# Optimization experiments

Measured on AMD Instinct MI355X. Metric: run time of the kernel, lower is better.

## Reference

```python
import jax, jax.numpy as jnp
from jax import lax
import numpy as np

B, N, S, K = 8, 4096, 1024, 32
D_FEAT = 64
EPS = 1e-5


def fps_idx(pts, npoint):
    # pts: [N,3] -> farthest point sampling indices [npoint] (deterministic start at 0)
    n = pts.shape[0]
    def body(i, state):
        dist, far, idxs = state
        idxs = idxs.at[i].set(far)
        d = jnp.sum((pts - pts[far]) ** 2, axis=-1)
        dist = jnp.minimum(dist, d)
        return dist, jnp.argmax(dist).astype(jnp.int32), idxs
    init = (jnp.full((n,), 1e10, pts.dtype), jnp.int32(0), jnp.zeros((npoint,), jnp.int32))
    _, _, idxs = lax.fori_loop(0, npoint, body, init)
    return idxs


def bn(x, g, b, axes, c_axis):
    # batch-norm, training mode (batch statistics), matching torch default module state
    m = jnp.mean(x, axes, keepdims=True)
    v = jnp.var(x, axes, keepdims=True)
    shape = [1] * x.ndim
    shape[c_axis] = -1
    return g.reshape(shape) * (x - m) * lax.rsqrt(v + EPS) + b.reshape(shape)


def conv1x1(x, w, b):
    # x: [B,C,S,K], w: [O,C], b: [O]
    return jnp.einsum('oc,bcsk->bosk', w, x) + b[None, :, None, None]


def setup_inputs():
    key = jax.random.key(0)
    ks = jax.random.split(key, 20)
    p = lambda k, shape: jax.random.normal(k, shape, jnp.float32) * 0.05
    inp = {
        'xyz': jax.random.normal(ks[0], (B, 3, N), jnp.float32),
        'features': jax.random.normal(ks[1], (B, D_FEAT, N), jnp.float32),
        # main MLP: 67 -> 64 -> 64 -> 128
        'w0': p(ks[2], (64, 67)), 'b0': p(ks[3], (64,)), 'g0': jnp.ones(64), 'be0': jnp.zeros(64),
        'w1': p(ks[4], (64, 64)), 'b1': p(ks[5], (64,)), 'g1': jnp.ones(64), 'be1': jnp.zeros(64),
        'w2': p(ks[6], (128, 64)), 'b2': p(ks[7], (128,)), 'g2': jnp.ones(128), 'be2': jnp.zeros(128),
        # WeightNet: 3 -> 8 -> 8 -> 16
        'ww0': p(ks[8], (8, 3)), 'wb0': p(ks[9], (8,)), 'wg0': jnp.ones(8), 'wbe0': jnp.zeros(8),
        'ww1': p(ks[10], (8, 8)), 'wb1': p(ks[11], (8,)), 'wg1': jnp.ones(8), 'wbe1': jnp.zeros(8),
        'ww2': p(ks[12], (16, 8)), 'wb2': p(ks[13], (16,)), 'wg2': jnp.ones(16), 'wbe2': jnp.zeros(16),
        # final linear 16*128 -> 128 and BN1d
        'lw': p(ks[14], (128, 16 * 128)), 'lb': p(ks[15], (128,)),
        'lg': jnp.ones(128), 'lbe': jnp.zeros(128),
    }
    return inp


def reference(xyz, features, w0, b0, g0, be0, w1, b1, g1, be1, w2, b2, g2, be2,
              ww0, wb0, wg0, wbe0, ww1, wb1, wg1, wbe1, ww2, wb2, wg2, wbe2,
              lw, lb, lg, lbe):
    xyz_t = jnp.transpose(xyz, (0, 2, 1))          # [B,N,3]
    feat_t = jnp.transpose(features, (0, 2, 1))    # [B,N,D]

    # farthest point sampling (indices non-differentiable, as in CUDA FPS)
    fidx = jax.vmap(lambda pts: fps_idx(pts, S))(lax.stop_gradient(xyz_t))  # [B,S]
    fps_xyz = jnp.take_along_axis(xyz_t, fidx[..., None], axis=1)           # [B,S,3]

    # KNN: squared distances [B,S,N], take K smallest
    d2 = (jnp.sum(fps_xyz ** 2, -1, keepdims=True)
          + jnp.sum(xyz_t ** 2, -1)[:, None, :]
          - 2.0 * jnp.einsum('bsc,bnc->bsn', fps_xyz, xyz_t))
    _, idx = lax.top_k(-lax.stop_gradient(d2), K)                            # [B,S,K]

    gather = jax.vmap(lambda src, i: src[i])
    grouped_xyz = gather(xyz_t, idx) - fps_xyz[:, :, None, :]                # [B,S,K,3]
    grouped_feat = gather(feat_t, idx)                                       # [B,S,K,D]
    nf = jnp.concatenate([grouped_xyz, grouped_feat], axis=-1)               # [B,S,K,3+D]

    nf = jnp.transpose(nf, (0, 3, 1, 2))                                     # [B,C,S,K]
    for w, b, g, be in ((w0, b0, g0, be0), (w1, b1, g1, be1), (w2, b2, g2, be2)):
        nf = jax.nn.relu(bn(conv1x1(nf, w, b), g, be, (0, 2, 3), 1))

    gx = jnp.transpose(grouped_xyz, (0, 3, 1, 2))                            # [B,3,S,K]
    wts = gx
    for w, b, g, be in ((ww0, wb0, wg0, wbe0), (ww1, wb1, wg1, wbe1), (ww2, wb2, wg2, wbe2)):
        wts = jax.nn.relu(bn(conv1x1(wts, w, b), g, be, (0, 2, 3), 1))       # [B,16,S,K]

    agg = jnp.einsum('bdsk,bcsk->bsdc', nf, wts)                             # [B,S,128,16]
    agg = agg.reshape(agg.shape[0], agg.shape[1], -1)                        # [B,S,2048] (D outer, C inner)
    lin = agg @ lw.T + lb                                                    # [B,S,128]
    lin = jnp.transpose(lin, (0, 2, 1))                                      # [B,128,S]
    out_f = jax.nn.relu(bn(lin, lg, lbe, (0, 2), 1))

    new_xyz = jnp.transpose(fps_xyz, (0, 2, 1))                              # [B,3,S]
    return (new_xyz, out_f)
```

## Files before the change

### kernel.cpp

```cpp
#include <hip/hip_runtime.h>
#include <hip/hip_bf16.h>

#define BB 8
#define NN 4096
#define SS 1024
#define KK 32
#define PP (BB*SS*KK)

typedef unsigned long long u64;
typedef unsigned int u32;
typedef unsigned short u16;
typedef float f32x2 __attribute__((ext_vector_type(2)));
typedef float f32x4 __attribute__((ext_vector_type(4)));
typedef short bf16x8 __attribute__((ext_vector_type(8)));

#define ST_Y0 0
#define ST_W0 64
#define ST_Y1 72
#define ST_W1 136
#define ST_Y2 144
#define ST_W2 272
#define ST_LIN 288

static __device__ __forceinline__ float bf2f(u32 u){ return __uint_as_float(u<<16); }
static __device__ __forceinline__ u16 f2bf(float f){ u32 u=__float_as_uint(f); return (u16)((u + 0x7FFFu + ((u>>16)&1u))>>16); }

static __device__ __forceinline__ f32x2 pk_add(f32x2 a, f32x2 b){
  f32x2 d; asm("v_pk_add_f32 %0, %1, %2" : "=v"(d) : "v"(a), "v"(b)); return d;
}
static __device__ __forceinline__ f32x2 pk_mul(f32x2 a, f32x2 b){
  f32x2 d; asm("v_pk_mul_f32 %0, %1, %2" : "=v"(d) : "v"(a), "v"(b)); return d;
}

static __device__ __forceinline__ f32x4 mfma16(bf16x8 a, bf16x8 b, f32x4 c){
  return __builtin_amdgcn_mfma_f32_16x16x32_bf16(a,b,c,0,0,0);
}

static __device__ __forceinline__ uint4 pack8(const float* v){
  uint4 r;
  r.x=(u32)f2bf(v[0])|((u32)f2bf(v[1])<<16);
  r.y=(u32)f2bf(v[2])|((u32)f2bf(v[3])<<16);
  r.z=(u32)f2bf(v[4])|((u32)f2bf(v[5])<<16);
  r.w=(u32)f2bf(v[6])|((u32)f2bf(v[7])<<16);
  return r;
}

static __device__ __forceinline__ void unp8_aff(uint4 r, const float* A, const float* C, int cb, float* o){
  o[0]=fmaxf(fmaf(bf2f(r.x&0xffffu),A[cb+0],C[cb+0]),0.f);
  o[1]=fmaxf(fmaf(bf2f(r.x>>16)    ,A[cb+1],C[cb+1]),0.f);
  o[2]=fmaxf(fmaf(bf2f(r.y&0xffffu),A[cb+2],C[cb+2]),0.f);
  o[3]=fmaxf(fmaf(bf2f(r.y>>16)    ,A[cb+3],C[cb+3]),0.f);
  o[4]=fmaxf(fmaf(bf2f(r.z&0xffffu),A[cb+4],C[cb+4]),0.f);
  o[5]=fmaxf(fmaf(bf2f(r.z>>16)    ,A[cb+5],C[cb+5]),0.f);
  o[6]=fmaxf(fmaf(bf2f(r.w&0xffffu),A[cb+6],C[cb+6]),0.f);
  o[7]=fmaxf(fmaf(bf2f(r.w>>16)    ,A[cb+7],C[cb+7]),0.f);
}

template<int CTRL, int RMASK>
static __device__ __forceinline__ u32 dppmax(u32 m){
  u32 t=(u32)__builtin_amdgcn_update_dpp(0, (int)m, CTRL, RMASK, 0xf, false);
  return t>m ? t : m;
}
template<int CTRL, int RMASK>
static __device__ __forceinline__ float dppadd1(float v){
  float t=__uint_as_float((u32)__builtin_amdgcn_update_dpp(0,(int)__float_as_uint(v),CTRL,RMASK,0xf,false));
  return v+t;
}
static __device__ __forceinline__ float dppsum(float v){
  v=dppadd1<0x111,0xf>(v);
  v=dppadd1<0x112,0xf>(v);
  v=dppadd1<0x114,0xf>(v);
  v=dppadd1<0x118,0xf>(v);
  v=dppadd1<0x142,0xa>(v);
  v=dppadd1<0x143,0xc>(v);
  return v;
}
static __device__ __forceinline__ float rl63(float v){
  return __uint_as_float((u32)__builtin_amdgcn_readlane((int)__float_as_uint(v),63));
}

__global__ __launch_bounds__(256) void k_featT(const float* __restrict__ f, float* __restrict__ ft,
    const float* __restrict__ w0,const float* __restrict__ ww0,
    float* __restrict__ w0t,float* __restrict__ wt0,float* __restrict__ wt1,float* __restrict__ wt2,
    const float* __restrict__ ww1,const float* __restrict__ ww2,
    float* __restrict__ statsf){
  __shared__ float tile[64][65];
  if (blockIdx.x==512){
    int t=threadIdx.x;
    for (int i=t;i<1024;i+=256) statsf[i]=0.f;
    for (int i=t;i<64*67;i+=256){ int o=i/67,k=i%67; w0t[k*64+o]=w0[i]; }
    for (int i=t;i<8*3;i+=256){ int o=i/3,k=i%3; wt0[k*8+o]=ww0[i]; }
    for (int i=t;i<8*8;i+=256){ int o=i>>3,k=i&7; wt1[k*8+o]=ww1[i]; }
    for (int i=t;i<16*8;i+=256){ int o=i>>3,k=i&7; wt2[k*16+o]=ww2[i]; }
    return;
  }
  int b=blockIdx.x>>6; int n0=(blockIdx.x&63)*64;
  const float* fb=f+(size_t)b*64*NN;
  int c0=threadIdx.x>>6, nn=threadIdx.x&63;
  #pragma unroll
  for (int it=0;it<16;it++){ int c=c0+it*4; tile[c][nn]=fb[(size_t)c*NN+n0+nn]; }
  __syncthreads();
  int cc=threadIdx.x&63, n1=threadIdx.x>>6;
  float* fo=ft+((size_t)b*NN+n0)*64;
  #pragma unroll
  for (int it=0;it<16;it++){ int n=n1+it*4; fo[(size_t)n*64+cc]=tile[cc][n]; }
}

__global__ __launch_bounds__(512) void k_fps(const float* __restrict__ xyz,
                                             float* __restrict__ fpsq, float* __restrict__ outx){
  __shared__ float X[NN], Y[NN], Z[NN];
  __shared__ float QX[SS], QY[SS], QZ[SS];
  __shared__ u64 red[2][8];
  int b=blockIdx.x, t=threadIdx.x;
  const float* xb=xyz+(size_t)b*3*NN;
  for (int i=t;i<NN;i+=512){ X[i]=xb[i]; Y[i]=xb[NN+i]; Z[i]=xb[2*NN+i]; }
  __syncthreads();
  f32x2 px[4],py[4],pz[4],dd[4];
  #pragma unroll
  for (int k=0;k<4;k++){
    int i=t*8+2*k;
    px[k].x=X[i]; px[k].y=X[i+1];
    py[k].x=Y[i]; py[k].y=Y[i+1];
    pz[k].x=Z[i]; pz[k].y=Z[i+1];
    dd[k].x=1e10f; dd[k].y=1e10f;
  }
  int wv=t>>6, ln=t&63;
  int far=0;
  for (int s=0;s<SS;s++){
    float fx=X[far], fy=Y[far], fz=Z[far];
    if (t==0){ QX[s]=fx; QY[s]=fy; QZ[s]=fz; }
    f32x2 nfx, nfy, nfz;
    nfx.x=-fx; nfx.y=-fx; nfy.x=-fy; nfy.y=-fy; nfz.x=-fz; nfz.y=-fz;
    #pragma unroll
    for (int k=0;k<4;k++){
      f32x2 dx=pk_add(px[k],nfx);
      f32x2 xx=pk_mul(dx,dx);
      f32x2 dy=pk_add(py[k],nfy);
      f32x2 yy=pk_mul(dy,dy);
      f32x2 dz=pk_add(pz[k],nfz);
      f32x2 zz=pk_mul(dz,dz);
      f32x2 s1=pk_add(xx,yy);
      f32x2 d2=pk_add(s1,zz);
      dd[k].x=fminf(dd[k].x,d2.x);
      dd[k].y=fminf(dd[k].y,d2.y);
    }
    float m01=fmaxf(dd[0].x,dd[0].y), m23=fmaxf(dd[1].x,dd[1].y);
    float m45=fmaxf(dd[2].x,dd[2].y), m67=fmaxf(dd[3].x,dd[3].y);
    u32 m=__float_as_uint(fmaxf(fmaxf(m01,m23),fmaxf(m45,m67)));
    m=dppmax<0x111,0xf>(m);
    m=dppmax<0x112,0xf>(m);
    m=dppmax<0x114,0xf>(m);
    m=dppmax<0x118,0xf>(m);
    u32 r15=(u32)__builtin_amdgcn_readlane((int)m,15);
    u32 r31=(u32)__builtin_amdgcn_readlane((int)m,31);
    u32 r47=(u32)__builtin_amdgcn_readlane((int)m,47);
    u32 r63=(u32)__builtin_amdgcn_readlane((int)m,63);
    u32 ab = r15>r31 ? r15 : r31;
    u32 cd = r47>r63 ? r47 : r63;
    u32 wmax = ab>cd ? ab : cd;
    int lj=8;
    if (__float_as_uint(dd[3].y)==wmax) lj=7;
    if (__float_as_uint(dd[3].x)==wmax) lj=6;
    if (__float_as_uint(dd[2].y)==wmax) lj=5;
    if (__float_as_uint(dd[2].x)==wmax) lj=4;
    if (__float_as_uint(dd[1].y)==wmax) lj=3;
    if (__float_as_uint(dd[1].x)==wmax) lj=2;
    if (__float_as_uint(dd[0].y)==wmax) lj=1;
    if (__float_as_uint(dd[0].x)==wmax) lj=0;
    u64 ball=__ballot(lj<8);
    u32 wl=(u32)__builtin_ctzll(ball);
    int gi=t*8+lj;
    u32 widx=(u32)__builtin_amdgcn_readlane(gi,wl);
    int pb=s&1;
    if (ln==0) red[pb][wv]=((u64)wmax<<32)|(u32)(4095u-widx);
    __syncthreads();
    const double* rd=(const double*)&red[pb][0];
    double g=fmax(fmax(fmax(rd[0],rd[1]),fmax(rd[2],rd[3])),
                  fmax(fmax(rd[4],rd[5]),fmax(rd[6],rd[7])));
    far=4095-(int)(__double_as_longlong(g)&0xFFFull);
  }
  __syncthreads();
  for (int i=t;i<SS;i+=512){
    float qx=QX[i], qy=QY[i], qz=QZ[i];
    float* q=&fpsq[((size_t)b*SS+i)*3]; q[0]=qx; q[1]=qy; q[2]=qz;
    outx[b*3*SS+i]=qx; outx[b*3*SS+SS+i]=qy; outx[b*3*SS+2*SS+i]=qz;
  }
}

#define KSTR 68
__global__ __launch_bounds__(512) void k_knn(const float* __restrict__ xyz, const float* __restrict__ fpsq,
                                             int* __restrict__ kidx){
  extern __shared__ char smem[];
  float* xs=(float*)smem;
  float* ys=xs+64*KSTR;
  float* zs=ys+64*KSTR;
  float* pn=zs+64*KSTR;
  int blk=blockIdx.x; int b=blk>>7; int s0=(blk&127)*8;
  const float* xb=xyz+(size_t)b*3*NN;
  for (int i=threadIdx.x;i<NN;i+=512){
    float x=xb[i],y=xb[NN+i],z=xb[2*NN+i];
    int slot=(i>>6)*KSTR+(i&63);
    xs[slot]=x; ys[slot]=y; zs[slot]=z;
    pn[slot]=__fadd_rn(__fadd_rn(__fmul_rn(x,x),__fmul_rn(y,y)),__fmul_rn(z,z));
  }
  __syncthreads();
  int wv=threadIdx.x>>6, ln=threadIdx.x&63;
  int s=s0+wv;
  const float* q=&fpsq[((size_t)b*SS+s)*3];
  float qx=q[0],qy=q[1],qz=q[2];
  float qn=__fadd_rn(__fadd_rn(__fmul_rn(qx,qx),__fmul_rn(qy,qy)),__fmul_rn(qz,qz));
  f32x2 qxx,qyy,qzz,qnn,mtwo;
  qxx.x=qx;qxx.y=qx; qyy.x=qy;qyy.y=qy; qzz.x=qz;qzz.y=qz; qnn.x=qn;qnn.y=qn;
  mtwo.x=-2.f; mtwo.y=-2.f;
  const float4* Xp=(const float4*)(xs+ln*KSTR);
  const float4* Yp=(const float4*)(ys+ln*KSTR);
  const float4* Zp=(const float4*)(zs+ln*KSTR);
  const float4* Pp=(const float4*)(pn+ln*KSTR);
  int base=ln*64;
  u64 v[64];
  #pragma unroll
  for (int g=0;g<16;g++){
    float4 x4=Xp[g], y4=Yp[g], z4=Zp[g], p4=Pp[g];
    #pragma unroll
    for (int h=0;h<2;h++){
      f32x2 px2,py2,pz2,pn2;
      if (h==0){ px2.x=x4.x;px2.y=x4.y; py2.x=y4.x;py2.y=y4.y; pz2.x=z4.x;pz2.y=z4.y; pn2.x=p4.x;pn2.y=p4.y; }
      else     { px2.x=x4.z;px2.y=x4.w; py2.x=y4.z;py2.y=y4.w; pz2.x=z4.z;pz2.y=z4.w; pn2.x=p4.z;pn2.y=p4.w; }
      f32x2 m1=pk_mul(qxx,px2);
      f32x2 mm=pk_mul(qyy,py2);
      f32x2 a1=pk_add(m1,mm);
      f32x2 m3=pk_mul(qzz,pz2);
      f32x2 dt=pk_add(a1,m3);
      f32x2 qp=pk_add(qnn,pn2);
      f32x2 nd=pk_mul(dt,mtwo);
      f32x2 d2=pk_add(qp,nd);
      #pragma unroll
      for (int e=0;e<2;e++){
        u32 bu=__float_as_uint(e?d2.y:d2.x);
        bu = ((int)bu<0)? ~bu : (bu|0x80000000u);
        v[g*4+h*2+e]=((u64)bu<<32)|(u32)(base+g*4+h*2+e);
      }
    }
  }
  u64 cand[8];
  #pragma unroll
  for (int gg=0;gg<8;gg++){
    u64 c=v[gg*8];
    #pragma unroll
    for (int j=1;j<8;j++){ u64 x=v[gg*8+j]; c = x<c?x:c; }
    cand[gg]=c;
  }
  u64 best=cand[0];
  #pragma unroll
  for (int gg=1;gg<8;gg++){ u64 x=cand[gg]; best = x<best?x:best; }
  int my=0;
  #pragma unroll 1
  for (int r=0;r<KK;r++){
    u64 w=best;
    #pragma unroll
    for (int m=1;m<64;m<<=1){ u64 o=__shfl_xor(w,m,64); w = o<w?o:w; }
    if (ln==r) my=(int)(w&0xFFFull);
    if (best==w){
      #pragma unroll
      for (int gg=0;gg<8;gg++){
        if (cand[gg]==w){
          u64 c=~0ull;
          #pragma unroll
          for (int j=0;j<8;j++){ u64 x=v[gg*8+j]; x = x>w ? x : ~0ull; c = x<c?x:c; }
          cand[gg]=c;
        }
      }
      u64 nb=cand[0];
      #pragma unroll
      for (int gg=1;gg<8;gg++){ u64 x=cand[gg]; nb = x<nb?x:nb; }
      best=nb;
    }
  }
  if (ln<KK) kidx[(((size_t)b*SS+s)<<5)+ln]=my;
}

__global__ __launch_bounds__(256) void k_l0(const float* __restrict__ xyz, const float* __restrict__ ft,
    const float* __restrict__ fpsq, const int* __restrict__ kidx,
    const float* __restrict__ w0t, const float* __restrict__ wt0,
    u16* __restrict__ y0, float* __restrict__ wl0, float* __restrict__ statsf){
  __shared__ u16 ytile[256][64];
  __shared__ float pS[4][64], pQ[4][64];
  __shared__ float pWS[4][8], pWQ[4][8];
  int t=threadIdx.x; int wv=t>>6, ln=t&63;
  int p=blockIdx.x*256+t;
  int b=p>>15;
  int site=p>>5;
  int j=kidx[p];
  const float* xb=xyz+(size_t)b*3*NN;
  const float* q=fpsq+(size_t)site*3;
  float gx=xb[j]-q[0], gy=xb[NN+j]-q[1], gz=xb[2*NN+j]-q[2];
  float acc[64];
  #pragma unroll
  for (int c=0;c<64;c++) acc[c]=fmaf(gx,w0t[c],fmaf(gy,w0t[64+c],gz*w0t[128+c]));
  const float4* fr=(const float4*)(ft+((size_t)b*NN+j)*64);
  #pragma unroll 1
  for (int kb=0;kb<4;kb++){
    float4 r0=fr[kb*4+0], r1=fr[kb*4+1], r2=fr[kb*4+2], r3=fr[kb*4+3];
    float ch[16]={r0.x,r0.y,r0.z,r0.w,r1.x,r1.y,r1.z,r1.w,r2.x,r2.y,r2.z,r2.w,r3.x,r3.y,r3.z,r3.w};
    const float* wb=w0t+(3+kb*16)*64;
    #pragma unroll
    for (int kk=0;kk<16;kk++){
      #pragma unroll
      for (int c=0;c<64;c++) acc[c]=fmaf(ch[kk],wb[kk*64+c],acc[c]);
    }
  }
  u16* yr=y0+(size_t)p*64;
  #pragma unroll
  for (int c8=0;c8<8;c8++){
    uint4 pk=pack8(&acc[c8*8]);
    ((uint4*)yr)[c8]=pk;
    *((uint4*)&ytile[t][c8*8])=pk;
  }
  float wa[8];
  #pragma unroll
  for (int o=0;o<8;o++) wa[o]=fmaf(gx,wt0[o],fmaf(gy,wt0[8+o],gz*wt0[16+o]));
  float4* wr=(float4*)(wl0+(size_t)p*8);
  wr[0]=make_float4(wa[0],wa[1],wa[2],wa[3]);
  wr[1]=make_float4(wa[4],wa[5],wa[6],wa[7]);
  float wS[8],wQ[8];
  #pragma unroll
  for (int o=0;o<8;o++){
    wS[o]=rl63(dppsum(wa[o]));
    wQ[o]=rl63(dppsum(wa[o]*wa[o]));
  }
  if (ln==0){
    #pragma unroll
    for (int o=0;o<8;o++){ pWS[wv][o]=wS[o]; pWQ[wv][o]=wQ[o]; }
  }
  __syncthreads();
  {
    int c=t&63, rg=t>>6;
    float S=0.f,Q=0.f;
    #pragma unroll 16
    for (int r=0;r<64;r++){
      float v=bf2f((u32)ytile[rg*64+r][c]);
      S+=v; Q=fmaf(v,v,Q);
    }
    pS[rg][c]=S; pQ[rg][c]=Q;
  }
  __syncthreads();
  if (t<64){
    float S=pS[0][t]+pS[1][t]+pS[2][t]+pS[3][t];
    float Q=pQ[0][t]+pQ[1][t]+pQ[2][t]+pQ[3][t];
    atomicAdd(&statsf[2*(ST_Y0+t)],S); atomicAdd(&statsf[2*(ST_Y0+t)+1],Q);
  } else if (t<72){
    int c=t-64;
    float S=pWS[0][c]+pWS[1][c]+pWS[2][c]+pWS[3][c];
    float Q=pWQ[0][c]+pWQ[1][c]+pWQ[2][c]+pWQ[3][c];
    atomicAdd(&statsf[2*(ST_W0+c)],S); atomicAdd(&statsf[2*(ST_W0+c)+1],Q);
  }
}

__global__ __launch_bounds__(256) void k_l1(const u16* __restrict__ y0, const float* __restrict__ wl0,
    const float* __restrict__ w1, const float* __restrict__ wt1,
    const float* __restrict__ statsf,
    const float* __restrict__ g0v, const float* __restrict__ be0v,
    const float* __restrict__ wg0v, const float* __restrict__ wbe0v,
    u16* __restrict__ y1, float* __restrict__ wl1, float* __restrict__ statso){
  __shared__ float A0[64],C0[64],AW[8],CW[8];
  __shared__ u16 Bw[64*72];
  __shared__ u16 Atile[4][16*72];
  __shared__ float pS[4][64], pQ[4][64];
  __shared__ float pWS[4][8], pWQ[4][8];
  int t=threadIdx.x; int wv=t>>6, ln=t&63;
  if (t<64){
    float sm=statsf[(ST_Y0+t)*2], sq=statsf[(ST_Y0+t)*2+1];
    float mean=sm*(1.f/PP), var=fmaxf(sq*(1.f/PP)-mean*mean,0.f);
    float a=g0v[t]*rsqrtf(var+1e-5f); A0[t]=a; C0[t]=be0v[t]-mean*a;
  } else if (t<72){
    int c=t-64;
    float sm=statsf[(ST_W0+c)*2], sq=statsf[(ST_W0+c)*2+1];
    float mean=sm*(1.f/PP), var=fmaxf(sq*(1.f/PP)-mean*mean,0.f);
    float a=wg0v[c]*rsqrtf(var+1e-5f); AW[c]=a; CW[c]=wbe0v[c]-mean*a;
  }
  for (int i=t;i<4096;i+=256){ Bw[(i>>6)*72+(i&63)]=f2bf(w1[i]); }
  __syncthreads();
  bf16x8 bfr[4][2];
  #pragma unroll
  for (int n=0;n<4;n++){
    const u16* bp=&Bw[(size_t)(n*16+(ln&15))*72 + (ln>>4)*8];
    bfr[n][0]=*(const bf16x8*)bp;
    bfr[n][1]=*(const bf16x8*)(bp+32);
  }
  float sS[4]={0,0,0,0}, sQ[4]={0,0,0,0};
  int p0=blockIdx.x*256 + wv*64;
  u16* At=Atile[wv];
  #pragma unroll 1
  for (int rs=0;rs<4;rs++){
    int pr=p0+rs*16;
    {
      const u16* ysrc=y0+(size_t)pr*64 + ln*16;
      uint4 raw0=*(const uint4*)ysrc;
      uint4 raw1=*(const uint4*)(ysrc+8);
      int row=ln>>2, cb=(ln&3)*16;
      float tmp[8];
      unp8_aff(raw0,A0,C0,cb,tmp);
      *(uint4*)&At[row*72+cb]=pack8(tmp);
      unp8_aff(raw1,A0,C0,cb+8,tmp);
      *(uint4*)&At[row*72+cb+8]=pack8(tmp);
    }
    const u16* ap=&At[(ln&15)*72 + (ln>>4)*8];
    bf16x8 a0=*(const bf16x8*)ap;
    bf16x8 a1=*(const bf16x8*)(ap+32);
    #pragma unroll
    for (int n=0;n<4;n++){
      f32x4 acc={0.f,0.f,0.f,0.f};
      acc=mfma16(a0,bfr[n][0],acc);
      acc=mfma16(a1,bfr[n][1],acc);
      #pragma unroll
      for (int i=0;i<4;i++){
        int row=(ln>>4)*4+i;
        y1[(size_t)(pr+row)*64 + n*16 + (ln&15)]=f2bf(acc[i]);
        sS[n]+=acc[i]; sQ[n]=fmaf(acc[i],acc[i],sQ[n]);
      }
    }
  }
  #pragma unroll
  for (int n=0;n<4;n++){
    sS[n]+=__shfl_xor(sS[n],16,64); sS[n]+=__shfl_xor(sS[n],32,64);
    sQ[n]+=__shfl_xor(sQ[n],16,64); sQ[n]+=__shfl_xor(sQ[n],32,64);
  }
  if (ln<16){
    #pragma unroll
    for (int n=0;n<4;n++){ pS[wv][n*16+ln]=sS[n]; pQ[wv][n*16+ln]=sQ[n]; }
  }
  int p=blockIdx.x*256+t;
  const float4* wvp=(const float4*)(wl0+(size_t)p*8);
  float4 v0=wvp[0], v1=wvp[1];
  float wi[8]={v0.x,v0.y,v0.z,v0.w,v1.x,v1.y,v1.z,v1.w};
  float wo[8];
  #pragma unroll
  for (int o=0;o<8;o++) wo[o]=0.f;
  #pragma unroll
  for (int k=0;k<8;k++){
    float xr=fmaxf(fmaf(wi[k],AW[k],CW[k]),0.f);
    #pragma unroll
    for (int o=0;o<8;o++) wo[o]=fmaf(xr,wt1[k*8+o],wo[o]);
  }
  float4* wr=(float4*)(wl1+(size_t)p*8);
  wr[0]=make_float4(wo[0],wo[1],wo[2],wo[3]);
  wr[1]=make_float4(wo[4],wo[5],wo[6],wo[7]);
  float wS[8],wQ[8];
  #pragma unroll
  for (int o=0;o<8;o++){
    wS[o]=rl63(dppsum(wo[o]));
    wQ[o]=rl63(dppsum(wo[o]*wo[o]));
  }
  if (ln==0){
    #pragma unroll
    for (int o=0;o<8;o++){ pWS[wv][o]=wS[o]; pWQ[wv][o]=wQ[o]; }
  }
  __syncthreads();
  if (t<64){
    float S=pS[0][t]+pS[1][t]+pS[2][t]+pS[3][t];
    float Q=pQ[0][t]+pQ[1][t]+pQ[2][t]+pQ[3][t];
    atomicAdd(&statso[2*(ST_Y1+t)],S); atomicAdd(&statso[2*(ST_Y1+t)+1],Q);
  } else if (t<72){
    int c=t-64;
    float S=pWS[0][c]+pWS[1][c]+pWS[2][c]+pWS[3][c];
    float Q=pWQ[0][c]+pWQ[1][c]+pWQ[2][c]+pWQ[3][c];
    atomicAdd(&statso[2*(ST_W1+c)],S); atomicAdd(&statso[2*(ST_W1+c)+1],Q);
  }
}

__global__ __launch_bounds__(256) void k_l2(const u16* __restrict__ y1, const float* __restrict__ wl1,
    const float* __restrict__ w2, const float* __restrict__ wt2,
    const float* __restrict__ statsf,
    const float* __restrict__ g1v, const float* __restrict__ be1v,
    const float* __restrict__ wg1v, const float* __restrict__ wbe1v,
    u16* __restrict__ y2, float* __restrict__ wl2, float* __restrict__ statso){
  __shared__ float A1[64],C1[64],AW[8],CW[8];
  __shared__ u16 Bw[128*72];
  __shared__ u16 Atile[4][16*72];
  __shared__ float pS[4][128], pQ[4][128];
  __shared__ float pWS[4][16], pWQ[4][16];
  int t=threadIdx.x; int wv=t>>6, ln=t&63;
  if (t<64){
    float sm=statsf[(ST_Y1+t)*2], sq=statsf[(ST_Y1+t)*2+1];
    float mean=sm*(1.f/PP), var=fmaxf(sq*(1.f/PP)-mean*mean,0.f);
    float a=g1v[t]*rsqrtf(var+1e-5f); A1[t]=a; C1[t]=be1v[t]-mean*a;
  } else if (t<72){
    int c=t-64;
    float sm=statsf[(ST_W1+c)*2], sq=statsf[(ST_W1+c)*2+1];
    float mean=sm*(1.f/PP), var=fmaxf(sq*(1.f/PP)-mean*mean,0.f);
    float a=wg1v[c]*rsqrtf(var+1e-5f); AW[c]=a; CW[c]=wbe1v[c]-mean*a;
  }
  for (int i=t;i<8192;i+=256){ Bw[(i>>6)*72+(i&63)]=f2bf(w2[i]); }
  __syncthreads();
  float sS[8]={0,0,0,0,0,0,0,0}, sQ[8]={0,0,0,0,0,0,0,0};
  int p0=blockIdx.x*256 + wv*64;
  u16* At=Atile[wv];
  #pragma unroll 1
  for (int rs=0;rs<4;rs++){
    int pr=p0+rs*16;
    {
      const u16* ysrc=y1+(size_t)pr*64 + ln*16;
      uint4 raw0=*(const uint4*)ysrc;
      uint4 raw1=*(const uint4*)(ysrc+8);
      int row=ln>>2, cb=(ln&3)*16;
      float tmp[8];
      unp8_aff(raw0,A1,C1,cb,tmp);
      *(uint4*)&At[row*72+cb]=pack8(tmp);
      unp8_aff(raw1,A1,C1,cb+8,tmp);
      *(uint4*)&At[row*72+cb+8]=pack8(tmp);
    }
    const u16* ap=&At[(ln&15)*72 + (ln>>4)*8];
    bf16x8 a0=*(const bf16x8*)ap;
    bf16x8 a1=*(const bf16x8*)(ap+32);
    #pragma unroll
    for (int n=0;n<8;n++){
      const u16* bp=&Bw[(size_t)(n*16+(ln&15))*72 + (ln>>4)*8];
      bf16x8 b0=*(const bf16x8*)bp;
      bf16x8 b1=*(const bf16x8*)(bp+32);
      f32x4 acc={0.f,0.f,0.f,0.f};
      acc=mfma16(a0,b0,acc);
      acc=mfma16(a1,b1,acc);
      #pragma unroll
      for (int i=0;i<4;i++){
        int row=(ln>>4)*4+i;
        y2[(size_t)(pr+row)*128 + n*16 + (ln&15)]=f2bf(acc[i]);
        sS[n]+=acc[i]; sQ[n]=fmaf(acc[i],acc[i],sQ[n]);
      }
    }
  }
  #pragma unroll
  for (int n=0;n<8;n++){
    sS[n]+=__shfl_xor(sS[n],16,64); sS[n]+=__shfl_xor(sS[n],32,64);
    sQ[n]+=__shfl_xor(sQ[n],16,64); sQ[n]+=__shfl_xor(sQ[n],32,64);
  }
  if (ln<16){
    #pragma unroll
    for (int n=0;n<8;n++){ pS[wv][n*16+ln]=sS[n]; pQ[wv][n*16+ln]=sQ[n]; }
  }
  int p=blockIdx.x*256+t;
  const float4* wvp=(const float4*)(wl1+(size_t)p*8);
  float4 v0=wvp[0], v1=wvp[1];
  float wi[8]={v0.x,v0.y,v0.z,v0.w,v1.x,v1.y,v1.z,v1.w};
  float wo[16];
  #pragma unroll
  for (int o=0;o<16;o++) wo[o]=0.f;
  #pragma unroll
  for (int k=0;k<8;k++){
    float xr=fmaxf(fmaf(wi[k],AW[k],CW[k]),0.f);
    #pragma unroll
    for (int o=0;o<16;o++) wo[o]=fmaf(xr,wt2[k*16+o],wo[o]);
  }
  float4* wr=(float4*)(wl2+(size_t)p*16);
  wr[0]=make_float4(wo[0],wo[1],wo[2],wo[3]);
  wr[1]=make_float4(wo[4],wo[5],wo[6],wo[7]);
  wr[2]=make_float4(wo[8],wo[9],wo[10],wo[11]);
  wr[3]=make_float4(wo[12],wo[13],wo[14],wo[15]);
  float wS[16],wQ[16];
  #pragma unroll
  for (int o=0;o<16;o++){
    wS[o]=rl63(dppsum(wo[o]));
    wQ[o]=rl63(dppsum(wo[o]*wo[o]));
  }
  if (ln==0){
    #pragma unroll
    for (int o=0;o<16;o++){ pWS[wv][o]=wS[o]; pWQ[wv][o]=wQ[o]; }
  }
  __syncthreads();
  if (t<128){
    float S=pS[0][t]+pS[1][t]+pS[2][t]+pS[3][t];
    float Q=pQ[0][t]+pQ[1][t]+pQ[2][t]+pQ[3][t];
    atomicAdd(&statso[2*(ST_Y2+t)],S); atomicAdd(&statso[2*(ST_Y2+t)+1],Q);
  } else if (t<144){
    int c=t-128;
    float S=pWS[0][c]+pWS[1][c]+pWS[2][c]+pWS[3][c];
    float Q=pWQ[0][c]+pWQ[1][c]+pWQ[2][c]+pWQ[3][c];
    atomicAdd(&statso[2*(ST_W2+c)],S); atomicAdd(&statso[2*(ST_W2+c)+1],Q);
  }
}

__global__ __launch_bounds__(256) void k_agg(const u16* __restrict__ y2, const float* __restrict__ wl2,
    const float* __restrict__ statsf,
    const float* __restrict__ g2v, const float* __restrict__ be2v,
    const float* __restrict__ wg2v, const float* __restrict__ wbe2v,
    u16* __restrict__ agg){
  __shared__ float A2[128],C2[128],AW[16],CW[16];
  __shared__ float nf[32*128];
  __shared__ float wt[32*16];
  int site=blockIdx.x; int t=threadIdx.x;
  if (t<128){
    float sm=statsf[(ST_Y2+t)*2], sq=statsf[(ST_Y2+t)*2+1];
    float mean=sm*(1.f/PP), var=fmaxf(sq*(1.f/PP)-mean*mean,0.f);
    float a=g2v[t]*rsqrtf(var+1e-5f); A2[t]=a; C2[t]=be2v[t]-mean*a;
  } else if (t<144){
    int c=t-128;
    float sm=statsf[(ST_W2+c)*2], sq=statsf[(ST_W2+c)*2+1];
    float mean=sm*(1.f/PP), var=fmaxf(sq*(1.f/PP)-mean*mean,0.f);
    float a=wg2v[c]*rsqrtf(var+1e-5f); AW[c]=a; CW[c]=wbe2v[c]-mean*a;
  }
  __syncthreads();
  const uint4* src=(const uint4*)(y2+(size_t)site*32*128);
  #pragma unroll
  for (int it=0;it<2;it++){
    int idx=t+it*256;
    uint4 r=src[idx];
    int base=(idx*8)&127; int kq=(idx*8)>>7;
    unp8_aff(r,A2,C2,base,&nf[kq*128+base]);
  }
  #pragma unroll
  for (int it=0;it<2;it++){
    int i=t+it*256;
    float x=wl2[(size_t)site*512+i]; int c=i&15;
    wt[i]=fmaxf(fmaf(x,AW[c],CW[c]),0.f);
  }
  __syncthreads();
  int d=t>>1, cb=(t&1)*8;
  float acc[8];
  #pragma unroll
  for (int e=0;e<8;e++) acc[e]=0.f;
  #pragma unroll 4
  for (int kq=0;kq<32;kq++){
    float nv=nf[kq*128+d];
    #pragma unroll
    for (int e=0;e<8;e++) acc[e]=fmaf(nv,wt[kq*16+cb+e],acc[e]);
  }
  ((uint4*)(agg+(size_t)site*2048))[t]=pack8(acc);
}

__global__ __launch_bounds__(256) void k_lin(const u16* __restrict__ agg, const float* __restrict__ lw,
                                             float* __restrict__ lin, float* __restrict__ outst){
  __shared__ float As[16][33];
  __shared__ float Bs[32][128];
  __shared__ float stS[8][132], stQ[8][132];
  int s0=blockIdx.x*16; int t=threadIdx.x;
  int tx=t&31, ty=t>>5;
  float a0[4]={0.f,0.f,0.f,0.f}, a1[4]={0.f,0.f,0.f,0.f};
  for (int kb=0;kb<2048;kb+=32){
    {
      int row=t>>4, kc=(t&15)*2;
      u32 raw=*(const u32*)(agg+((size_t)(s0+row))*2048+kb+kc);
      As[row][kc]=bf2f(raw&0xffffu); As[row][kc+1]=bf2f(raw>>16);
    }
    {
      int o=t>>1, ks=(t&1)*16;
      const float* lr=lw+(size_t)o*2048+kb+ks;
      #pragma unroll
      for (int i=0;i<16;i+=4){
        float4 r=*(const float4*)(lr+i);
        Bs[ks+i][o]=r.x; Bs[ks+i+1][o]=r.y; Bs[ks+i+2][o]=r.z; Bs[ks+i+3][o]=r.w;
      }
    }
    __syncthreads();
    #pragma unroll 8
    for (int kk=0;kk<32;kk++){
      float av0=As[ty*2][kk], av1=As[ty*2+1][kk];
      float4 bv=*(const float4*)(&Bs[kk][tx*4]);
      a0[0]=fmaf(av0,bv.x,a0[0]); a0[1]=fmaf(av0,bv.y,a0[1]);
      a0[2]=fmaf(av0,bv.z,a0[2]); a0[3]=fmaf(av0,bv.w,a0[3]);
      a1[0]=fmaf(av1,bv.x,a1[0]); a1[1]=fmaf(av1,bv.y,a1[1]);
      a1[2]=fmaf(av1,bv.z,a1[2]); a1[3]=fmaf(av1,bv.w,a1[3]);
    }
    __syncthreads();
  }
  *(float4*)(lin+((size_t)(s0+ty*2  ))*128+tx*4)=make_float4(a0[0],a0[1],a0[2],a0[3]);
  *(float4*)(lin+((size_t)(s0+ty*2+1))*128+tx*4)=make_float4(a1[0],a1[1],a1[2],a1[3]);
  #pragma unroll
  for (int j=0;j<4;j++){
    stS[ty][tx*4+j]=a0[j]+a1[j];
    stQ[ty][tx*4+j]=fmaf(a1[j],a1[j],a0[j]*a0[j]);
  }
  __syncthreads();
  if (t<128){
    float S=0.f,Q=0.f;
    #pragma unroll
    for (int k=0;k<8;k++){ S+=stS[k][t]; Q+=stQ[k][t]; }
    atomicAdd(&outst[2*t],S); atomicAdd(&outst[2*t+1],Q);
  }
}

__global__ __launch_bounds__(256) void k_out(const float* __restrict__ lin, const float* __restrict__ statsf,
    const float* __restrict__ lg, const float* __restrict__ lbe, float* __restrict__ outf){
  int t=blockIdx.x*256+threadIdx.x;
  int s4=(t&255)*4; int o=(t>>8)&127; int b=t>>15;
  float sm=statsf[(ST_LIN+o)*2], sq=statsf[(ST_LIN+o)*2+1];
  float mean=sm*(1.f/8192.f), var=fmaxf(sq*(1.f/8192.f)-mean*mean,0.f);
  float a=lg[o]*rsqrtf(var+1e-5f), cc=lbe[o]-mean*a;
  float v0=lin[((size_t)b*SS+s4+0)*128+o];
  float v1=lin[((size_t)b*SS+s4+1)*128+o];
  float v2=lin[((size_t)b*SS+s4+2)*128+o];
  float v3=lin[((size_t)b*SS+s4+3)*128+o];
  float4 r=make_float4(fmaxf(fmaf(v0,a,cc),0.f),fmaxf(fmaf(v1,a,cc),0.f),
                       fmaxf(fmaf(v2,a,cc),0.f),fmaxf(fmaf(v3,a,cc),0.f));
  *(float4*)(outf+((size_t)b*128+o)*SS+s4)=r;
}

extern "C" void kernel_launch(void* const* d_in, const int* in_sizes, int n_in,
                              void* d_out, int out_size, void* d_ws, size_t ws_size,
                              hipStream_t stream){
  (void)in_sizes;(void)n_in;(void)out_size;(void)ws_size;
  const float* xyz =(const float*)d_in[0];
  const float* feat=(const float*)d_in[1];
  const float* w0=(const float*)d_in[2];  const float* g0=(const float*)d_in[4];  const float* be0=(const float*)d_in[5];
  const float* w1=(const float*)d_in[6];  const float* g1=(const float*)d_in[8];  const float* be1=(const float*)d_in[9];
  const float* w2=(const float*)d_in[10]; const float* g2=(const float*)d_in[12]; const float* be2=(const float*)d_in[13];
  const float* ww0=(const float*)d_in[14]; const float* wg0=(const float*)d_in[16]; const float* wbe0=(const float*)d_in[17];
  const float* ww1=(const float*)d_in[18]; const float* wg1=(const float*)d_in[20]; const float* wbe1=(const float*)d_in[21];
  const float* ww2=(const float*)d_in[22]; const float* wg2=(const float*)d_in[24]; const float* wbe2=(const float*)d_in[25];
  const float* lw=(const float*)d_in[26]; const float* lg=(const float*)d_in[28]; const float* lbe=(const float*)d_in[29];
  float* out=(float*)d_out;
  char* ws=(char*)d_ws;

  size_t cur=0;
  auto alloc=[&](size_t bytes)->size_t{ cur=(cur+255)&~(size_t)255; size_t o=cur; cur+=bytes; return o; };
  size_t o_stats=alloc(4096);
  size_t o_w0t =alloc(67*64*4);
  size_t o_wt0 =alloc(3*8*4);
  size_t o_wt1 =alloc(8*8*4);
  size_t o_wt2 =alloc(8*16*4);
  size_t o_fpsq=alloc((size_t)BB*SS*3*4);
  size_t o_kidx=alloc((size_t)PP*4);
  size_t o_ft  =alloc((size_t)BB*NN*64*4);
  size_t o_y0  =alloc((size_t)PP*64*2);
  size_t o_y1  =alloc((size_t)PP*64*2);
  size_t o_y2  =alloc((size_t)PP*128*2);
  size_t o_wl0 =alloc((size_t)PP*8*4);
  size_t o_wl1 =alloc((size_t)PP*8*4);
  size_t o_wl2 =alloc((size_t)PP*16*4);
  size_t o_agg =alloc((size_t)8192*2048*2);
  size_t o_lin =alloc((size_t)8192*128*4);

  float* statsf=(float*)(ws+o_stats);
  float* w0t=(float*)(ws+o_w0t);
  float* wt0=(float*)(ws+o_wt0); float* wt1=(float*)(ws+o_wt1); float* wt2=(float*)(ws+o_wt2);
  float* fpsq=(float*)(ws+o_fpsq); int* kidx=(int*)(ws+o_kidx);
  float* ft=(float*)(ws+o_ft);
  u16* y0=(u16*)(ws+o_y0); u16* y1=(u16*)(ws+o_y1); u16* y2=(u16*)(ws+o_y2);
  float* wl0=(float*)(ws+o_wl0); float* wl1=(float*)(ws+o_wl1); float* wl2=(float*)(ws+o_wl2);
  u16* agg=(u16*)(ws+o_agg); float* lin=(float*)(ws+o_lin);

  size_t knn_smem = (size_t)4*64*KSTR*4;

  hipLaunchKernelGGL(k_featT,dim3(513),dim3(256),0,stream,feat,ft,
                     w0,ww0,w0t,wt0,wt1,wt2,ww1,ww2,statsf);
  hipLaunchKernelGGL(k_fps,dim3(BB),dim3(512),0,stream,xyz,fpsq,out);
  hipLaunchKernelGGL(k_knn,dim3(1024),dim3(512),knn_smem,stream,xyz,fpsq,kidx);
  hipLaunchKernelGGL(k_l0,dim3(PP/256),dim3(256),0,stream,xyz,ft,fpsq,kidx,w0t,wt0,y0,wl0,statsf);
  hipLaunchKernelGGL(k_l1,dim3(PP/256),dim3(256),0,stream,y0,wl0,w1,wt1,statsf,g0,be0,wg0,wbe0,y1,wl1,statsf);
  hipLaunchKernelGGL(k_l2,dim3(PP/256),dim3(256),0,stream,y1,wl1,w2,wt2,statsf,g1,be1,wg1,wbe1,y2,wl2,statsf);
  hipLaunchKernelGGL(k_agg,dim3(8192),dim3(256),0,stream,y2,wl2,statsf,g2,be2,wg2,wbe2,agg);
  hipLaunchKernelGGL(k_lin,dim3(512),dim3(256),0,stream,agg,lw,lin,statsf+2*ST_LIN);
  hipLaunchKernelGGL(k_out,dim3(1024),dim3(256),0,stream,lin,statsf,lg,lbe,out+BB*3*SS);
}
```

Measured before the change: 1.177 ms.

## Move layer-0 conv and final linear onto bf16 MFMA with converted weights

Layer 0 now computes the 64-channel feature projection with bf16 16x16 MFMA instructions, staging a bf16 copy of the weights in shared memory and adding the xyz terms in fp32. Its BN statistics come from lane shuffles instead of a shared-memory tile pass. The final 2048->128 linear also switches from an fp32 shared-memory SIMT GEMM to direct-from-global bf16 MFMA, using a bf16 copy of lw produced in the transpose kernel. This cuts FMA throughput cost but rounds features and the linear weights to bf16, and layer 0 now writes y0 as scattered 2-byte stores.

```diff
diff --git a/kernel.cpp b/kernel.cpp
--- a/kernel.cpp
+++ b/kernel.cpp
@@ -80,19 +80,22 @@
 }
 
 __global__ __launch_bounds__(256) void k_featT(const float* __restrict__ f, float* __restrict__ ft,
-    const float* __restrict__ w0,const float* __restrict__ ww0,
-    float* __restrict__ w0t,float* __restrict__ wt0,float* __restrict__ wt1,float* __restrict__ wt2,
-    const float* __restrict__ ww1,const float* __restrict__ ww2,
+    const float* __restrict__ ww0,const float* __restrict__ ww1,const float* __restrict__ ww2,
+    const float* __restrict__ lw, u16* __restrict__ lwbf,
+    float* __restrict__ wt0,float* __restrict__ wt1,float* __restrict__ wt2,
     float* __restrict__ statsf){
   __shared__ float tile[64][65];
   if (blockIdx.x==512){
     int t=threadIdx.x;
     for (int i=t;i<1024;i+=256) statsf[i]=0.f;
-    for (int i=t;i<64*67;i+=256){ int o=i/67,k=i%67; w0t[k*64+o]=w0[i]; }
     for (int i=t;i<8*3;i+=256){ int o=i/3,k=i%3; wt0[k*8+o]=ww0[i]; }
     for (int i=t;i<8*8;i+=256){ int o=i>>3,k=i&7; wt1[k*8+o]=ww1[i]; }
     for (int i=t;i<16*8;i+=256){ int o=i>>3,k=i&7; wt2[k*16+o]=ww2[i]; }
     return;
+  }
+  {
+    int base2=blockIdx.x*512;
+    for (int i=threadIdx.x;i<512;i+=256) lwbf[base2+i]=f2bf(lw[base2+i]);
   }
   int b=blockIdx.x>>6; int n0=(blockIdx.x&63)*64;
   const float* fb=f+(size_t)b*64*NN;
@@ -281,9 +284,11 @@
 
 __global__ __launch_bounds__(256) void k_l0(const float* __restrict__ xyz, const float* __restrict__ ft,
     const float* __restrict__ fpsq, const int* __restrict__ kidx,
-    const float* __restrict__ w0t, const float* __restrict__ wt0,
+    const float* __restrict__ w0, const float* __restrict__ wt0,
     u16* __restrict__ y0, float* __restrict__ wl0, float* __restrict__ statsf){
-  __shared__ u16 ytile[256][64];
+  __shared__ u16 Bw[64*72];
+  __shared__ float gt[256][4];
+  __shared__ int jt[256];
   __shared__ float pS[4][64], pQ[4][64];
   __shared__ float pWS[4][8], pWQ[4][8];
   int t=threadIdx.x; int wv=t>>6, ln=t&63;
@@ -294,27 +299,64 @@
   const float* xb=xyz+(size_t)b*3*NN;
   const float* q=fpsq+(size_t)site*3;
   float gx=xb[j]-q[0], gy=xb[NN+j]-q[1], gz=xb[2*NN+j]-q[2];
-  float acc[64];
-  #pragma unroll
-  for (int c=0;c<64;c++) acc[c]=fmaf(gx,w0t[c],fmaf(gy,w0t[64+c],gz*w0t[128+c]));
-  const float4* fr=(const float4*)(ft+((size_t)b*NN+j)*64);
+  gt[t][0]=gx; gt[t][1]=gy; gt[t][2]=gz; gt[t][3]=0.f; jt[t]=j;
+  for (int i=t;i<4096;i+=256){ int col=i>>6,k=i&63; Bw[col*72+k]=f2bf(w0[col*67+3+k]); }
+  __syncthreads();
+  float wxc[4],wyc[4],wzc[4];
+  #pragma unroll
+  for (int n=0;n<4;n++){
+    int c=n*16+(ln&15);
+    wxc[n]=w0[c*67+0]; wyc[n]=w0[c*67+1]; wzc[n]=w0[c*67+2];
+  }
+  float sS[4]={0,0,0,0}, sQ[4]={0,0,0,0};
+  int base=wv*64;
   #pragma unroll 1
-  for (int kb=0;kb<4;kb++){
-    float4 r0=fr[kb*4+0], r1=fr[kb*4+1], r2=fr[kb*4+2], r3=fr[kb*4+3];
-    float ch[16]={r0.x,r0.y,r0.z,r0.w,r1.x,r1.y,r1.z,r1.w,r2.x,r2.y,r2.z,r2.w,r3.x,r3.y,r3.z,r3.w};
-    const float* wb=w0t+(3+kb*16)*64;
-    #pragma unroll
-    for (int kk=0;kk<16;kk++){
+  for (int rs=0;rs<4;rs++){
+    int lrow=base+rs*16+(ln&15);
+    int jr=jt[lrow];
+    const float* fp=ft+((size_t)b*NN+jr)*64 + (ln>>4)*8;
+    float4 fa=*(const float4*)fp, fb4=*(const float4*)(fp+4);
+    float4 fc=*(const float4*)(fp+32), fd=*(const float4*)(fp+36);
+    float va[8]={fa.x,fa.y,fa.z,fa.w,fb4.x,fb4.y,fb4.z,fb4.w};
+    float vb[8]={fc.x,fc.y,fc.z,fc.w,fd.x,fd.y,fd.z,fd.w};
+    bf16x8 a0,a1;
+    #pragma unroll
+    for (int e=0;e<8;e++){ ((u16*)&a0)[e]=(short)f2bf(va[e]); ((u16*)&a1)[e]=(short)f2bf(vb[e]); }
+    int r0=base+rs*16+(ln>>4)*4;
+    float4 g0v4=*(const float4*)&gt[r0+0][0];
+    float4 g1v4=*(const float4*)&gt[r0+1][0];
+    float4 g2v4=*(const float4*)&gt[r0+2][0];
+    float4 g3v4=*(const float4*)&gt[r0+3][0];
+    float gxr[4]={g0v4.x,g1v4.x,g2v4.x,g3v4.x};
+    float gyr[4]={g0v4.y,g1v4.y,g2v4.y,g3v4.y};
+    float gzr[4]={g0v4.z,g1v4.z,g2v4.z,g3v4.z};
+    int pr=blockIdx.x*256+base+rs*16;
+    #pragma unroll
+    for (int n=0;n<4;n++){
+      const u16* bp=&Bw[(size_t)(n*16+(ln&15))*72 + (ln>>4)*8];
+      bf16x8 b0=*(const bf16x8*)bp;
+      bf16x8 b1=*(const bf16x8*)(bp+32);
+      f32x4 acc;
       #pragma unroll
-      for (int c=0;c<64;c++) acc[c]=fmaf(ch[kk],wb[kk*64+c],acc[c]);
+      for (int i=0;i<4;i++) acc[i]=fmaf(gxr[i],wxc[n],fmaf(gyr[i],wyc[n],gzr[i]*wzc[n]));
+      acc=mfma16(a0,b0,acc);
+      acc=mfma16(a1,b1,acc);
+      #pragma unroll
+      for (int i=0;i<4;i++){
+        int row=(ln>>4)*4+i;
+        y0[(size_t)(pr+row)*64 + n*16 + (ln&15)]=f2bf(acc[i]);
+        sS[n]+=acc[i]; sQ[n]=fmaf(acc[i],acc[i],sQ[n]);
+      }
     }
   }
-  u16* yr=y0+(size_t)p*64;
-  #pragma unroll
-  for (int c8=0;c8<8;c8++){
-    uint4 pk=pack8(&acc[c8*8]);
-    ((uint4*)yr)[c8]=pk;
-    *((uint4*)&ytile[t][c8*8])=pk;
+  #pragma unroll
+  for (int n=0;n<4;n++){
+    sS[n]+=__shfl_xor(sS[n],16,64); sS[n]+=__shfl_xor(sS[n],32,64);
+    sQ[n]+=__shfl_xor(sQ[n],16,64); sQ[n]+=__shfl_xor(sQ[n],32,64);
+  }
+  if (ln<16){
+    #pragma unroll
+    for (int n=0;n<4;n++){ pS[wv][n*16+ln]=sS[n]; pQ[wv][n*16+ln]=sQ[n]; }
   }
   float wa[8];
   #pragma unroll
@@ -331,17 +373,6 @@
   if (ln==0){
     #pragma unroll
     for (int o=0;o<8;o++){ pWS[wv][o]=wS[o]; pWQ[wv][o]=wQ[o]; }
-  }
-  __syncthreads();
-  {
-    int c=t&63, rg=t>>6;
-    float S=0.f,Q=0.f;
-    #pragma unroll 16
-    for (int r=0;r<64;r++){
-      float v=bf2f((u32)ytile[rg*64+r][c]);
-      S+=v; Q=fmaf(v,v,Q);
-    }
-    pS[rg][c]=S; pQ[rg][c]=Q;
   }
   __syncthreads();
   if (t<64){
@@ -626,53 +657,40 @@
   ((uint4*)(agg+(size_t)site*2048))[t]=pack8(acc);
 }
 
-__global__ __launch_bounds__(256) void k_lin(const u16* __restrict__ agg, const float* __restrict__ lw,
+__global__ __launch_bounds__(256) void k_lin(const u16* __restrict__ agg, const u16* __restrict__ lwbf,
                                              float* __restrict__ lin, float* __restrict__ outst){
-  __shared__ float As[16][33];
-  __shared__ float Bs[32][128];
-  __shared__ float stS[8][132], stQ[8][132];
-  int s0=blockIdx.x*16; int t=threadIdx.x;
-  int tx=t&31, ty=t>>5;
-  float a0[4]={0.f,0.f,0.f,0.f}, a1[4]={0.f,0.f,0.f,0.f};
+  __shared__ float pS[4][32], pQ[4][32];
+  int t=threadIdx.x; int wv=t>>6, ln=t&63;
+  int s0=blockIdx.x*16;
+  const u16* arow=agg+(size_t)(s0+(ln&15))*2048 + (ln>>4)*8;
+  const u16* b0p=lwbf+(size_t)(wv*32+(ln&15))*2048 + (ln>>4)*8;
+  const u16* b1p=b0p + (size_t)16*2048;
+  f32x4 acc0={0.f,0.f,0.f,0.f}, acc1={0.f,0.f,0.f,0.f};
+  #pragma unroll 4
   for (int kb=0;kb<2048;kb+=32){
-    {
-      int row=t>>4, kc=(t&15)*2;
-      u32 raw=*(const u32*)(agg+((size_t)(s0+row))*2048+kb+kc);
-      As[row][kc]=bf2f(raw&0xffffu); As[row][kc+1]=bf2f(raw>>16);
-    }
-    {
-      int o=t>>1, ks=(t&1)*16;
-      const float* lr=lw+(size_t)o*2048+kb+ks;
-      #pragma unroll
-      for (int i=0;i<16;i+=4){
-        float4 r=*(const float4*)(lr+i);
-        Bs[ks+i][o]=r.x; Bs[ks+i+1][o]=r.y; Bs[ks+i+2][o]=r.z; Bs[ks+i+3][o]=r.w;
-      }
-    }
-    __syncthreads();
-    #pragma unroll 8
-    for (int kk=0;kk<32;kk++){
-      float av0=As[ty*2][kk], av1=As[ty*2+1][kk];
-      float4 bv=*(const float4*)(&Bs[kk][tx*4]);
-      a0[0]=fmaf(av0,bv.x,a0[0]); a0[1]=fmaf(av0,bv.y,a0[1]);
-      a0[2]=fmaf(av0,bv.z,a0[2]); a0[3]=fmaf(av0,bv.w,a0[3]);
-      a1[0]=fmaf(av1,bv.x,a1[0]); a1[1]=fmaf(av1,bv.y,a1[1]);
-      a1[2]=fmaf(av1,bv.z,a1[2]); a1[3]=fmaf(av1,bv.w,a1[3]);
-    }
-    __syncthreads();
-  }
-  *(float4*)(lin+((size_t)(s0+ty*2  ))*128+tx*4)=make_float4(a0[0],a0[1],a0[2],a0[3]);
-  *(float4*)(lin+((size_t)(s0+ty*2+1))*128+tx*4)=make_float4(a1[0],a1[1],a1[2],a1[3]);
-  #pragma unroll
-  for (int j=0;j<4;j++){
-    stS[ty][tx*4+j]=a0[j]+a1[j];
-    stQ[ty][tx*4+j]=fmaf(a1[j],a1[j],a0[j]*a0[j]);
-  }
+    bf16x8 a=*(const bf16x8*)(arow+kb);
+    bf16x8 b0=*(const bf16x8*)(b0p+kb);
+    bf16x8 b1=*(const bf16x8*)(b1p+kb);
+    acc0=mfma16(a,b0,acc0);
+    acc1=mfma16(a,b1,acc1);
+  }
+  float sS0=0.f,sQ0=0.f,sS1=0.f,sQ1=0.f;
+  #pragma unroll
+  for (int i=0;i<4;i++){
+    int row=(ln>>4)*4+i;
+    lin[(size_t)(s0+row)*128 + wv*32 + (ln&15)]=acc0[i];
+    lin[(size_t)(s0+row)*128 + wv*32 + 16 + (ln&15)]=acc1[i];
+    sS0+=acc0[i]; sQ0=fmaf(acc0[i],acc0[i],sQ0);
+    sS1+=acc1[i]; sQ1=fmaf(acc1[i],acc1[i],sQ1);
+  }
+  sS0+=__shfl_xor(sS0,16,64); sS0+=__shfl_xor(sS0,32,64);
+  sQ0+=__shfl_xor(sQ0,16,64); sQ0+=__shfl_xor(sQ0,32,64);
+  sS1+=__shfl_xor(sS1,16,64); sS1+=__shfl_xor(sS1,32,64);
+  sQ1+=__shfl_xor(sQ1,16,64); sQ1+=__shfl_xor(sQ1,32,64);
+  if (ln<16){ pS[wv][ln]=sS0; pS[wv][16+ln]=sS1; pQ[wv][ln]=sQ0; pQ[wv][16+ln]=sQ1; }
   __syncthreads();
   if (t<128){
-    float S=0.f,Q=0.f;
-    #pragma unroll
-    for (int k=0;k<8;k++){ S+=stS[k][t]; Q+=stQ[k][t]; }
+    float S=pS[t>>5][t&31], Q=pQ[t>>5][t&31];
     atomicAdd(&outst[2*t],S); atomicAdd(&outst[2*t+1],Q);
   }
 }
@@ -712,10 +730,10 @@
   size_t cur=0;
   auto alloc=[&](size_t bytes)->size_t{ cur=(cur+255)&~(size_t)255; size_t o=cur; cur+=bytes; return o; };
   size_t o_stats=alloc(4096);
-  size_t o_w0t =alloc(67*64*4);
   size_t o_wt0 =alloc(3*8*4);
   size_t o_wt1 =alloc(8*8*4);
   size_t o_wt2 =alloc(8*16*4);
+  size_t o_lwbf=alloc((size_t)128*2048*2);
   size_t o_fpsq=alloc((size_t)BB*SS*3*4);
   size_t o_kidx=alloc((size_t)PP*4);
   size_t o_ft  =alloc((size_t)BB*NN*64*4);
@@ -729,8 +747,8 @@
   size_t o_lin =alloc((size_t)8192*128*4);
 
   float* statsf=(float*)(ws+o_stats);
-  float* w0t=(float*)(ws+o_w0t);
   float* wt0=(float*)(ws+o_wt0); float* wt1=(float*)(ws+o_wt1); float* wt2=(float*)(ws+o_wt2);
+  u16* lwbf=(u16*)(ws+o_lwbf);
   float* fpsq=(float*)(ws+o_fpsq); int* kidx=(int*)(ws+o_kidx);
   float* ft=(float*)(ws+o_ft);
   u16* y0=(u16*)(ws+o_y0); u16* y1=(u16*)(ws+o_y1); u16* y2=(u16*)(ws+o_y2);
@@ -740,13 +758,13 @@
   size_t knn_smem = (size_t)4*64*KSTR*4;
 
   hipLaunchKernelGGL(k_featT,dim3(513),dim3(256),0,stream,feat,ft,
-                     w0,ww0,w0t,wt0,wt1,wt2,ww1,ww2,statsf);
+                     ww0,ww1,ww2,lw,lwbf,wt0,wt1,wt2,statsf);
   hipLaunchKernelGGL(k_fps,dim3(BB),dim3(512),0,stream,xyz,fpsq,out);
   hipLaunchKernelGGL(k_knn,dim3(1024),dim3(512),knn_smem,stream,xyz,fpsq,kidx);
-  hipLaunchKernelGGL(k_l0,dim3(PP/256),dim3(256),0,stream,xyz,ft,fpsq,kidx,w0t,wt0,y0,wl0,statsf);
+  hipLaunchKernelGGL(k_l0,dim3(PP/256),dim3(256),0,stream,xyz,ft,fpsq,kidx,w0,wt0,y0,wl0,statsf);
   hipLaunchKernelGGL(k_l1,dim3(PP/256),dim3(256),0,stream,y0,wl0,w1,wt1,statsf,g0,be0,wg0,wbe0,y1,wl1,statsf);
   hipLaunchKernelGGL(k_l2,dim3(PP/256),dim3(256),0,stream,y1,wl1,w2,wt2,statsf,g1,be1,wg1,wbe1,y2,wl2,statsf);
   hipLaunchKernelGGL(k_agg,dim3(8192),dim3(256),0,stream,y2,wl2,statsf,g2,be2,wg2,wbe2,agg);
-  hipLaunchKernelGGL(k_lin,dim3(512),dim3(256),0,stream,agg,lw,lin,statsf+2*ST_LIN);
+  hipLaunchKernelGGL(k_lin,dim3(512),dim3(256),0,stream,agg,lwbf,lin,statsf+2*ST_LIN);
   hipLaunchKernelGGL(k_out,dim3(1024),dim3(256),0,stream,lin,statsf,lg,lbe,out+BB*3*SS);
 }
```

After: 1.096 ms. 6.9% less time.
